# Performance work log

Measured on AMD Instinct MI355X. Metric: run time of the kernel, lower is better.

## Reference

```python
import jax, jax.numpy as jnp
import numpy as np

RCR = 5.2          # radial cutoff
RCA = 3.5          # angular cutoff
ETA_R = 16.0
SHF_R = jnp.asarray(0.9 + 0.26875 * np.arange(16), jnp.float32)          # 16 radial shifts
ZETA = 32.0
SHF_Z = jnp.asarray((2 * np.arange(8) + 1) * np.pi / 16.0, jnp.float32)  # 8 angle shifts
ETA_A = 8.0
SHF_A = jnp.asarray(0.9 + 0.65 * np.arange(4), jnp.float32)              # 4 angular radial shifts
NUM_SPECIES = 4
NUM_PAIRS = NUM_SPECIES * (NUM_SPECIES + 1) // 2  # 10


def _pair_index_table():
    idx = np.zeros((NUM_SPECIES, NUM_SPECIES), np.int32)
    c = 0
    for s1 in range(NUM_SPECIES):
        for s2 in range(s1, NUM_SPECIES):
            idx[s1, s2] = c
            idx[s2, s1] = c
            c += 1
    return jnp.asarray(idx)

PAIR_IDX = _pair_index_table()


def _cutoff(d, rc):
    return jnp.where(d <= rc, 0.5 * jnp.cos(jnp.pi * d / rc) + 0.5, 0.0)


def setup_inputs() -> dict:
    key = jax.random.key(0)
    k1, k2 = jax.random.split(key)
    species = jax.random.randint(k1, (32, 48), 0, NUM_SPECIES, dtype=jnp.int32)
    coords = jax.random.uniform(k2, (32, 48, 3), jnp.float32) * 7.0  # 7 Angstrom box
    return {"species": species, "coords": coords}


def reference(species, coords):
    B, A = species.shape
    dt = coords.dtype
    # vec[b,i,j] = coords[j] - coords[i]
    diff = coords[:, None, :, :] - coords[:, :, None, :]           # [B,A,A,3]
    d2 = jnp.sum(diff * diff, -1)
    eye = jnp.eye(A, dtype=bool)
    dist = jnp.sqrt(jnp.where(eye, 1.0, d2))                        # safe on diagonal
    valid = (species[:, :, None] >= 0) & (species[:, None, :] >= 0) & (~eye)

    # ---------- radial AEV ----------
    fc_r = jnp.where(valid & (dist <= RCR), _cutoff(dist, RCR), 0.0)
    rad_terms = 0.25 * jnp.exp(-ETA_R * (dist[..., None] - SHF_R) ** 2) * fc_r[..., None]  # [B,A,A,16]
    sp_onehot = jax.nn.one_hot(jnp.clip(species, 0), NUM_SPECIES, dtype=dt)                # [B,A,4]
    radial = jnp.einsum('bijr,bjs->bisr', rad_terms, sp_onehot).reshape(B, A, NUM_SPECIES * 16)

    # ---------- angular AEV ----------
    in_ca = valid & (dist <= RCA)
    fc_a = jnp.where(in_ca, _cutoff(dist, RCA), 0.0)
    dotp = jnp.einsum('bijc,bikc->bijk', diff, diff)                # [B,A,A,A]
    cos_t = 0.95 * dotp / (dist[:, :, :, None] * dist[:, :, None, :])
    angles = jnp.arccos(cos_t)
    f1 = ((1.0 + jnp.cos(angles[..., None] - SHF_Z)) * 0.5) ** ZETA          # [B,A,A,A,8]
    avg_d = 0.5 * (dist[:, :, :, None] + dist[:, :, None, :])
    f2 = jnp.exp(-ETA_A * (avg_d[..., None] - SHF_A) ** 2)                   # [B,A,A,A,4]
    jk = jnp.triu(jnp.ones((A, A), bool), 1)                                 # unordered neighbor pairs j<k
    trip_mask = in_ca[:, :, :, None] & in_ca[:, :, None, :] & jk
    w = jnp.where(trip_mask, 2.0 * fc_a[:, :, :, None] * fc_a[:, :, None, :], 0.0)  # [B,A,A,A]
    pair_idx = PAIR_IDX[jnp.clip(species, 0)[:, :, None], jnp.clip(species, 0)[:, None, :]]  # [B,A,A]
    pair_oh = jax.nn.one_hot(pair_idx, NUM_PAIRS, dtype=dt)                  # [B,A,A,10]
    angular = jnp.einsum('bijk,bijka,bijkz,bjkp->bipaz', w, f2, f1, pair_oh)
    angular = angular.reshape(B, A, NUM_PAIRS * 4 * 8)

    aevs = jnp.concatenate([radial, angular], axis=-1)   # [B,A,384]
    return species, aevs
```

## Files before the change

kernel.cpp:

```cpp
#include <hip/hip_runtime.h>
#include <math.h>

#define NB 32
#define NA 48
#define RCRf 5.2f
#define RCAf 3.5f
#define PI_F 3.14159265358979f
#define TREC 1128

typedef unsigned short ushort_t;
typedef __fp16 h2f __attribute__((ext_vector_type(2)));

static __device__ __forceinline__ unsigned pkh(float a, float b) {
    h2f v = __builtin_amdgcn_cvt_pkrtz(a, b);
    return __builtin_bit_cast(unsigned, v);
}
static __device__ __forceinline__ float uph(ushort_t u) {
    return (float)__builtin_bit_cast(__fp16, u);
}

static __device__ __forceinline__ void tri_decode(int t, int m, int T, int& jj, int& kk) {
    const int u = T - 1 - t;
    int r = (int)((sqrtf(8.0f * (float)u + 1.0f) - 1.0f) * 0.5f);
    while (r * (r + 1) / 2 > u) --r;
    while ((r + 1) * (r + 2) / 2 <= u) ++r;
    jj = m - 2 - r;
    kk = m - 1 - (u - r * (r + 1) / 2);
}

__global__ __launch_bounds__(320)
void aev_kernel(const int* __restrict__ species, const float* __restrict__ coords,
                float* __restrict__ out)
{
    const int bid = blockIdx.x;
    const int b = bid / NA;
    const int i = bid - b * NA;
    const int tid = threadIdx.x;

    __shared__ float crd[NA * 3];
    __shared__ int   ssp[NA];
    __shared__ float pd[NA], pfr[NA];
    __shared__ __align__(16) float4 cpk[NA];
    __shared__ float cfc[NA];
    __shared__ int   csp[NA];
    __shared__ int   sm;
    __shared__ float radpart[5 * 64];
    __shared__ __align__(16) ushort_t f1h[TREC * 8];
    __shared__ __align__(16) ushort_t w2h[TREC * 4];
    __shared__ int   cnt[10];
    __shared__ unsigned cur[10];

    if (tid < NA * 3) crd[tid] = coords[(size_t)b * NA * 3 + tid];
    if (tid >= 192 && tid < 192 + NA) ssp[tid - 192] = species[b * NA + (tid - 192)];
    if (tid >= 256 && tid < 266) cnt[tid - 256] = 0;
    __syncthreads();

    const float xi = crd[3 * i], yi = crd[3 * i + 1], zi = crd[3 * i + 2];

    if (tid < 64) {
        const int j = tid;
        float dx = 0.f, dy = 0.f, dz = 0.f, d = 1.0f, fr = 0.0f, fa = 0.0f;
        bool inA = false;
        if (j < NA) {
            dx = crd[3 * j] - xi; dy = crd[3 * j + 1] - yi; dz = crd[3 * j + 2] - zi;
            d = sqrtf(dx * dx + dy * dy + dz * dz);
            if (j != i && d <= RCRf) fr = 0.5f * __cosf((PI_F / RCRf) * d) + 0.5f;
            if (j != i && d <= RCAf) { inA = true; fa = 0.5f * __cosf((PI_F / RCAf) * d) + 0.5f; }
            pd[j] = d; pfr[j] = fr;
        }
        const unsigned long long mask = __ballot(inA);
        if (inA) {
            const int pos = (int)__popcll(mask & ((1ull << j) - 1ull));
            cpk[pos] = make_float4(dx, dy, dz, d);
            cfc[pos] = fa; csp[pos] = ssp[j];
        }
        if (j == 0) sm = (int)__popcll(mask);
    }
    __syncthreads();

    const int m = sm;
    const int T = m * (m - 1) / 2;

    {
        const int f = tid & 63, seg = tid >> 6;
        const int s = f >> 4, r = f & 15;
        const float shf = 0.9f + 0.26875f * (float)r;
        float acc = 0.0f;
        const int j0 = seg * 10, j1 = min(NA, j0 + 10);
        for (int j = j0; j < j1; ++j) {
            const float fr = pfr[j];
            if (fr != 0.0f) {
                const float u = pd[j] - shf;
                const float v = 0.25f * __expf(-16.0f * u * u) * fr;
                acc += (ssp[j] == s) ? v : 0.0f;
            }
        }
        radpart[seg * 64 + f] = acc;
    }
    for (int t = tid; t < T; t += 320) {
        int jj, kk; tri_decode(t, m, T, jj, kk);
        const int s1 = csp[jj], s2 = csp[kk];
        const int lo = min(s1, s2), hi = max(s1, s2);
        const int p = (lo * (9 - lo)) / 2 + (hi - lo);
        atomicAdd(&cnt[p], 1);
    }
    __syncthreads();

    const int pmine = tid >> 5, amine = (tid >> 3) & 3, zmine = tid & 7;
    int mybase = 0, mycnt = 0, run = 0;
    #pragma unroll
    for (int p = 0; p < 10; ++p) {
        const int cp = cnt[p];
        if (p == pmine) { mybase = run; mycnt = cp; }
        if (tid < 10 && p == tid) cur[tid] = (unsigned)run;
        run += cp;
    }
    __syncthreads();

    const float CZ[8] = { 0.98078528f, 0.83146961f, 0.55557023f, 0.19509032f,
                         -0.19509032f,-0.55557023f,-0.83146961f,-0.98078528f };
    const float SZ[8] = { 0.19509032f, 0.55557023f, 0.83146961f, 0.98078528f,
                          0.98078528f, 0.83146961f, 0.55557023f, 0.19509032f };
    const float SA[4] = { 0.9f, 1.55f, 2.2f, 2.85f };

    for (int t = tid; t < T; t += 320) {
        int jj, kk; tri_decode(t, m, T, jj, kk);
        const float4 qj = cpk[jj];
        const float4 qk = cpk[kk];
        const float dot = qj.x * qk.x + qj.y * qk.y + qj.z * qk.z;
        const float cosT = 0.95f * dot * __frcp_rn(qj.w * qk.w);
        const float sinT = sqrtf(fmaxf(1.0f - cosT * cosT, 0.0f));
        const float avg = 0.5f * (qj.w + qk.w);
        const float w = 2.0f * cfc[jj] * cfc[kk];
        const int s1 = csp[jj], s2 = csp[kk];
        const int lo = min(s1, s2), hi = max(s1, s2);
        const int p = (lo * (9 - lo)) / 2 + (hi - lo);

        float f1v[8];
        #pragma unroll
        for (int z = 0; z < 8; ++z) {
            const float base = 0.5f + 0.5f * (cosT * CZ[z] + sinT * SZ[z]);
            const float b2 = base * base, b4 = b2 * b2, b8 = b4 * b4, b16 = b8 * b8;
            f1v[z] = b16 * b16;
        }
        float w2v[4];
        #pragma unroll
        for (int a = 0; a < 4; ++a) {
            const float u = avg - SA[a];
            w2v[a] = w * __expf(-8.0f * u * u);
        }
        const unsigned pos = atomicAdd(&cur[p], 1u);
        uint4 rf;
        rf.x = pkh(f1v[0], f1v[1]); rf.y = pkh(f1v[2], f1v[3]);
        rf.z = pkh(f1v[4], f1v[5]); rf.w = pkh(f1v[6], f1v[7]);
        ((uint4*)f1h)[pos] = rf;
        uint2 rw;
        rw.x = pkh(w2v[0], w2v[1]); rw.y = pkh(w2v[2], w2v[3]);
        ((uint2*)w2h)[pos] = rw;
    }
    __syncthreads();

    float acc_a = 0.0f;
    for (int k = mybase; k < mybase + mycnt; ++k)
        acc_a += uph(w2h[k * 4 + amine]) * uph(f1h[k * 8 + zmine]);

    float* op = out + NB * NA + (size_t)(b * NA + i) * 384;
    if (tid < 64) {
        op[tid] = radpart[tid] + radpart[64 + tid] + radpart[128 + tid] +
                  radpart[192 + tid] + radpart[256 + tid];
    }
    op[64 + tid] = acc_a;
    if (tid == 0) out[b * NA + i] = (float)ssp[i];
}

extern "C" void kernel_launch(void* const* d_in, const int* in_sizes, int n_in,
                              void* d_out, int out_size, void* d_ws, size_t ws_size,
                              hipStream_t stream) {
    const int*   species = (const int*)d_in[0];
    const float* coords  = (const float*)d_in[1];
    float*       out     = (float*)d_out;
    aev_kernel<<<NB * NA, 320, 0, stream>>>(species, coords, out);
}
```

Before: 66.03 us.

## Store compact per-triplet records and compute angular terms in consumer threads

The counting pass, prefix sum and atomic bucketing by species pair are removed. Each triplet now writes a compact record (cosT, sinT, fp16 avg/weight, pair id) indexed by triplet number. Each output thread scans every record and evaluates only those matching its pair, computing its own angle and radial term. Coordinates and species are also read straight from global memory instead of being staged in shared memory. This drops atomics and a barrier but makes every thread scan all T records. It also recomputes exp and the power chain per output element, and adds fp16 rounding of the average distance.

```diff
diff --git a/kernel.cpp b/kernel.cpp
--- a/kernel.cpp
+++ b/kernel.cpp
@@ -6,17 +6,12 @@
 #define RCRf 5.2f
 #define RCAf 3.5f
 #define PI_F 3.14159265358979f
-#define TREC 1128
+#define TREC 1081
 
-typedef unsigned short ushort_t;
 typedef __fp16 h2f __attribute__((ext_vector_type(2)));
-
 static __device__ __forceinline__ unsigned pkh(float a, float b) {
     h2f v = __builtin_amdgcn_cvt_pkrtz(a, b);
     return __builtin_bit_cast(unsigned, v);
-}
-static __device__ __forceinline__ float uph(ushort_t u) {
-    return (float)__builtin_bit_cast(__fp16, u);
 }
 
 static __device__ __forceinline__ void tri_decode(int t, int m, int T, int& jj, int& kk) {
@@ -37,42 +32,35 @@
     const int i = bid - b * NA;
     const int tid = threadIdx.x;
 
-    __shared__ float crd[NA * 3];
+    __shared__ float pd[NA], pfr[NA];
     __shared__ int   ssp[NA];
-    __shared__ float pd[NA], pfr[NA];
     __shared__ __align__(16) float4 cpk[NA];
     __shared__ float cfc[NA];
     __shared__ int   csp[NA];
     __shared__ int   sm;
     __shared__ float radpart[5 * 64];
-    __shared__ __align__(16) ushort_t f1h[TREC * 8];
-    __shared__ __align__(16) ushort_t w2h[TREC * 4];
-    __shared__ int   cnt[10];
-    __shared__ unsigned cur[10];
-
-    if (tid < NA * 3) crd[tid] = coords[(size_t)b * NA * 3 + tid];
-    if (tid >= 192 && tid < 192 + NA) ssp[tid - 192] = species[b * NA + (tid - 192)];
-    if (tid >= 256 && tid < 266) cnt[tid - 256] = 0;
-    __syncthreads();
-
-    const float xi = crd[3 * i], yi = crd[3 * i + 1], zi = crd[3 * i + 2];
+    __shared__ __align__(16) uint4 rec[TREC];
 
     if (tid < 64) {
         const int j = tid;
         float dx = 0.f, dy = 0.f, dz = 0.f, d = 1.0f, fr = 0.0f, fa = 0.0f;
+        int sj = 0;
         bool inA = false;
         if (j < NA) {
-            dx = crd[3 * j] - xi; dy = crd[3 * j + 1] - yi; dz = crd[3 * j + 2] - zi;
+            const float* cb = coords + (size_t)b * NA * 3;
+            const float xi = cb[3 * i], yi = cb[3 * i + 1], zi = cb[3 * i + 2];
+            dx = cb[3 * j] - xi; dy = cb[3 * j + 1] - yi; dz = cb[3 * j + 2] - zi;
             d = sqrtf(dx * dx + dy * dy + dz * dz);
+            sj = species[b * NA + j];
             if (j != i && d <= RCRf) fr = 0.5f * __cosf((PI_F / RCRf) * d) + 0.5f;
             if (j != i && d <= RCAf) { inA = true; fa = 0.5f * __cosf((PI_F / RCAf) * d) + 0.5f; }
-            pd[j] = d; pfr[j] = fr;
+            pd[j] = d; pfr[j] = fr; ssp[j] = sj;
         }
         const unsigned long long mask = __ballot(inA);
         if (inA) {
             const int pos = (int)__popcll(mask & ((1ull << j) - 1ull));
             cpk[pos] = make_float4(dx, dy, dz, d);
-            cfc[pos] = fa; csp[pos] = ssp[j];
+            cfc[pos] = fa; csp[pos] = sj;
         }
         if (j == 0) sm = (int)__popcll(mask);
     }
@@ -97,31 +85,6 @@
         }
         radpart[seg * 64 + f] = acc;
     }
-    for (int t = tid; t < T; t += 320) {
-        int jj, kk; tri_decode(t, m, T, jj, kk);
-        const int s1 = csp[jj], s2 = csp[kk];
-        const int lo = min(s1, s2), hi = max(s1, s2);
-        const int p = (lo * (9 - lo)) / 2 + (hi - lo);
-        atomicAdd(&cnt[p], 1);
-    }
-    __syncthreads();
-
-    const int pmine = tid >> 5, amine = (tid >> 3) & 3, zmine = tid & 7;
-    int mybase = 0, mycnt = 0, run = 0;
-    #pragma unroll
-    for (int p = 0; p < 10; ++p) {
-        const int cp = cnt[p];
-        if (p == pmine) { mybase = run; mycnt = cp; }
-        if (tid < 10 && p == tid) cur[tid] = (unsigned)run;
-        run += cp;
-    }
-    __syncthreads();
-
-    const float CZ[8] = { 0.98078528f, 0.83146961f, 0.55557023f, 0.19509032f,
-                         -0.19509032f,-0.55557023f,-0.83146961f,-0.98078528f };
-    const float SZ[8] = { 0.19509032f, 0.55557023f, 0.83146961f, 0.98078528f,
-                          0.98078528f, 0.83146961f, 0.55557023f, 0.19509032f };
-    const float SA[4] = { 0.9f, 1.55f, 2.2f, 2.85f };
 
     for (int t = tid; t < T; t += 320) {
         int jj, kk; tri_decode(t, m, T, jj, kk);
@@ -135,34 +98,36 @@
         const int s1 = csp[jj], s2 = csp[kk];
         const int lo = min(s1, s2), hi = max(s1, s2);
         const int p = (lo * (9 - lo)) / 2 + (hi - lo);
-
-        float f1v[8];
-        #pragma unroll
-        for (int z = 0; z < 8; ++z) {
-            const float base = 0.5f + 0.5f * (cosT * CZ[z] + sinT * SZ[z]);
-            const float b2 = base * base, b4 = b2 * b2, b8 = b4 * b4, b16 = b8 * b8;
-            f1v[z] = b16 * b16;
-        }
-        float w2v[4];
-        #pragma unroll
-        for (int a = 0; a < 4; ++a) {
-            const float u = avg - SA[a];
-            w2v[a] = w * __expf(-8.0f * u * u);
-        }
-        const unsigned pos = atomicAdd(&cur[p], 1u);
-        uint4 rf;
-        rf.x = pkh(f1v[0], f1v[1]); rf.y = pkh(f1v[2], f1v[3]);
-        rf.z = pkh(f1v[4], f1v[5]); rf.w = pkh(f1v[6], f1v[7]);
-        ((uint4*)f1h)[pos] = rf;
-        uint2 rw;
-        rw.x = pkh(w2v[0], w2v[1]); rw.y = pkh(w2v[2], w2v[3]);
-        ((uint2*)w2h)[pos] = rw;
+        uint4 r;
+        r.x = __float_as_uint(cosT);
+        r.y = __float_as_uint(sinT);
+        r.z = pkh(avg, w);
+        r.w = (unsigned)p;
+        rec[t] = r;
     }
     __syncthreads();
 
+    const int pmine = tid >> 5;
+    const float CZt[8] = { 0.98078528f, 0.83146961f, 0.55557023f, 0.19509032f,
+                          -0.19509032f,-0.55557023f,-0.83146961f,-0.98078528f };
+    const float SZt[8] = { 0.19509032f, 0.55557023f, 0.83146961f, 0.98078528f,
+                           0.98078528f, 0.83146961f, 0.55557023f, 0.19509032f };
+    const float cz = CZt[tid & 7], sz = SZt[tid & 7];
+    const float sa = 0.9f + 0.65f * (float)((tid >> 3) & 3);
     float acc_a = 0.0f;
-    for (int k = mybase; k < mybase + mycnt; ++k)
-        acc_a += uph(w2h[k * 4 + amine]) * uph(f1h[k * 8 + zmine]);
+    for (int t = 0; t < T; ++t) {
+        const uint4 r = rec[t];
+        if ((int)r.w == pmine) {
+            const float cosT = __uint_as_float(r.x);
+            const float sinT = __uint_as_float(r.y);
+            const h2f aw = __builtin_bit_cast(h2f, r.z);
+            const float avg = (float)aw.x, w = (float)aw.y;
+            const float base = 0.5f + 0.5f * (cosT * cz + sinT * sz);
+            const float b2 = base * base, b4 = b2 * b2, b8 = b4 * b4, b16 = b8 * b8;
+            const float u = avg - sa;
+            acc_a += w * __expf(-8.0f * u * u) * (b16 * b16);
+        }
+    }
 
     float* op = out + NB * NA + (size_t)(b * NA + i) * 384;
     if (tid < 64) {
```

Result: slower. 88.22 us (+33.6%).

## Chunk triplet staging buffer and load coords directly from global

Applied to the files above, without the earlier changes.

The per-block LDS staging buffer for triplet features now has a fixed size and is processed in chunks, so a neighbour count of any size no longer overflows it. The smaller buffer also lowers LDS use per block, which may let more blocks share a CU. The initial copy of coordinates and species into LDS, and the barrier after it, are removed; each thread reads its own values straight from global memory. Multi-chunk cases add extra barriers and a second counting pass.

```diff
diff --git a/kernel.cpp b/kernel.cpp
--- a/kernel.cpp
+++ b/kernel.cpp
@@ -6,11 +6,10 @@
 #define RCRf 5.2f
 #define RCAf 3.5f
 #define PI_F 3.14159265358979f
-#define TREC 1128
+#define CMAX 1000
 
 typedef unsigned short ushort_t;
 typedef __fp16 h2f __attribute__((ext_vector_type(2)));
-
 static __device__ __forceinline__ unsigned pkh(float a, float b) {
     h2f v = __builtin_amdgcn_cvt_pkrtz(a, b);
     return __builtin_bit_cast(unsigned, v);
@@ -37,42 +36,40 @@
     const int i = bid - b * NA;
     const int tid = threadIdx.x;
 
-    __shared__ float crd[NA * 3];
+    __shared__ float pd[NA], pfr[NA];
     __shared__ int   ssp[NA];
-    __shared__ float pd[NA], pfr[NA];
     __shared__ __align__(16) float4 cpk[NA];
     __shared__ float cfc[NA];
     __shared__ int   csp[NA];
     __shared__ int   sm;
     __shared__ float radpart[5 * 64];
-    __shared__ __align__(16) ushort_t f1h[TREC * 8];
-    __shared__ __align__(16) ushort_t w2h[TREC * 4];
+    __shared__ __align__(16) ushort_t f1h[CMAX * 8];
+    __shared__ __align__(16) ushort_t w2h[CMAX * 4];
     __shared__ int   cnt[10];
     __shared__ unsigned cur[10];
 
-    if (tid < NA * 3) crd[tid] = coords[(size_t)b * NA * 3 + tid];
-    if (tid >= 192 && tid < 192 + NA) ssp[tid - 192] = species[b * NA + (tid - 192)];
     if (tid >= 256 && tid < 266) cnt[tid - 256] = 0;
-    __syncthreads();
-
-    const float xi = crd[3 * i], yi = crd[3 * i + 1], zi = crd[3 * i + 2];
 
     if (tid < 64) {
         const int j = tid;
         float dx = 0.f, dy = 0.f, dz = 0.f, d = 1.0f, fr = 0.0f, fa = 0.0f;
+        int sj = 0;
         bool inA = false;
         if (j < NA) {
-            dx = crd[3 * j] - xi; dy = crd[3 * j + 1] - yi; dz = crd[3 * j + 2] - zi;
+            const float* cb = coords + (size_t)b * NA * 3;
+            const float xi = cb[3 * i], yi = cb[3 * i + 1], zi = cb[3 * i + 2];
+            dx = cb[3 * j] - xi; dy = cb[3 * j + 1] - yi; dz = cb[3 * j + 2] - zi;
             d = sqrtf(dx * dx + dy * dy + dz * dz);
+            sj = species[b * NA + j];
             if (j != i && d <= RCRf) fr = 0.5f * __cosf((PI_F / RCRf) * d) + 0.5f;
             if (j != i && d <= RCAf) { inA = true; fa = 0.5f * __cosf((PI_F / RCAf) * d) + 0.5f; }
-            pd[j] = d; pfr[j] = fr;
+            pd[j] = d; pfr[j] = fr; ssp[j] = sj;
         }
         const unsigned long long mask = __ballot(inA);
         if (inA) {
             const int pos = (int)__popcll(mask & ((1ull << j) - 1ull));
             cpk[pos] = make_float4(dx, dy, dz, d);
-            cfc[pos] = fa; csp[pos] = ssp[j];
+            cfc[pos] = fa; csp[pos] = sj;
         }
         if (j == 0) sm = (int)__popcll(mask);
     }
@@ -80,6 +77,7 @@
 
     const int m = sm;
     const int T = m * (m - 1) / 2;
+    const int nchunks = (T + CMAX - 1) / CMAX;
 
     {
         const int f = tid & 63, seg = tid >> 6;
@@ -97,72 +95,96 @@
         }
         radpart[seg * 64 + f] = acc;
     }
-    for (int t = tid; t < T; t += 320) {
-        int jj, kk; tri_decode(t, m, T, jj, kk);
-        const int s1 = csp[jj], s2 = csp[kk];
-        const int lo = min(s1, s2), hi = max(s1, s2);
-        const int p = (lo * (9 - lo)) / 2 + (hi - lo);
-        atomicAdd(&cnt[p], 1);
+    {
+        const int cT = min(CMAX, T);
+        for (int t = tid; t < cT; t += 320) {
+            int jj, kk; tri_decode(t, m, T, jj, kk);
+            const int s1 = csp[jj], s2 = csp[kk];
+            const int lo = min(s1, s2), hi = max(s1, s2);
+            const int p = (lo * (9 - lo)) / 2 + (hi - lo);
+            atomicAdd(&cnt[p], 1);
+        }
     }
     __syncthreads();
 
     const int pmine = tid >> 5, amine = (tid >> 3) & 3, zmine = tid & 7;
-    int mybase = 0, mycnt = 0, run = 0;
-    #pragma unroll
-    for (int p = 0; p < 10; ++p) {
-        const int cp = cnt[p];
-        if (p == pmine) { mybase = run; mycnt = cp; }
-        if (tid < 10 && p == tid) cur[tid] = (unsigned)run;
-        run += cp;
-    }
-    __syncthreads();
-
     const float CZ[8] = { 0.98078528f, 0.83146961f, 0.55557023f, 0.19509032f,
                          -0.19509032f,-0.55557023f,-0.83146961f,-0.98078528f };
     const float SZ[8] = { 0.19509032f, 0.55557023f, 0.83146961f, 0.98078528f,
                           0.98078528f, 0.83146961f, 0.55557023f, 0.19509032f };
     const float SA[4] = { 0.9f, 1.55f, 2.2f, 2.85f };
-
-    for (int t = tid; t < T; t += 320) {
-        int jj, kk; tri_decode(t, m, T, jj, kk);
-        const float4 qj = cpk[jj];
-        const float4 qk = cpk[kk];
-        const float dot = qj.x * qk.x + qj.y * qk.y + qj.z * qk.z;
-        const float cosT = 0.95f * dot * __frcp_rn(qj.w * qk.w);
-        const float sinT = sqrtf(fmaxf(1.0f - cosT * cosT, 0.0f));
-        const float avg = 0.5f * (qj.w + qk.w);
-        const float w = 2.0f * cfc[jj] * cfc[kk];
-        const int s1 = csp[jj], s2 = csp[kk];
-        const int lo = min(s1, s2), hi = max(s1, s2);
-        const int p = (lo * (9 - lo)) / 2 + (hi - lo);
-
-        float f1v[8];
+    float acc_a = 0.0f;
+
+    for (int c = 0; c < nchunks; ++c) {
+        const int t0 = c * CMAX;
+        const int cT = min(CMAX, T - t0);
+
+        int mybase = 0, mycnt = 0, run = 0;
         #pragma unroll
-        for (int z = 0; z < 8; ++z) {
-            const float base = 0.5f + 0.5f * (cosT * CZ[z] + sinT * SZ[z]);
-            const float b2 = base * base, b4 = b2 * b2, b8 = b4 * b4, b16 = b8 * b8;
-            f1v[z] = b16 * b16;
-        }
-        float w2v[4];
-        #pragma unroll
-        for (int a = 0; a < 4; ++a) {
-            const float u = avg - SA[a];
-            w2v[a] = w * __expf(-8.0f * u * u);
-        }
-        const unsigned pos = atomicAdd(&cur[p], 1u);
-        uint4 rf;
-        rf.x = pkh(f1v[0], f1v[1]); rf.y = pkh(f1v[2], f1v[3]);
-        rf.z = pkh(f1v[4], f1v[5]); rf.w = pkh(f1v[6], f1v[7]);
-        ((uint4*)f1h)[pos] = rf;
-        uint2 rw;
-        rw.x = pkh(w2v[0], w2v[1]); rw.y = pkh(w2v[2], w2v[3]);
-        ((uint2*)w2h)[pos] = rw;
-    }
-    __syncthreads();
-
-    float acc_a = 0.0f;
-    for (int k = mybase; k < mybase + mycnt; ++k)
-        acc_a += uph(w2h[k * 4 + amine]) * uph(f1h[k * 8 + zmine]);
+        for (int p = 0; p < 10; ++p) {
+            const int cp = cnt[p];
+            if (p == pmine) { mybase = run; mycnt = cp; }
+            if (tid < 10 && p == tid) cur[tid] = (unsigned)run;
+            run += cp;
+        }
+        __syncthreads();
+
+        for (int t = tid; t < cT; t += 320) {
+            int jj, kk; tri_decode(t0 + t, m, T, jj, kk);
+            const float4 qj = cpk[jj];
+            const float4 qk = cpk[kk];
+            const float dot = qj.x * qk.x + qj.y * qk.y + qj.z * qk.z;
+            const float cosT = 0.95f * dot * __frcp_rn(qj.w * qk.w);
+            const float sinT = sqrtf(fmaxf(1.0f - cosT * cosT, 0.0f));
+            const float avg = 0.5f * (qj.w + qk.w);
+            const float w = 2.0f * cfc[jj] * cfc[kk];
+            const int s1 = csp[jj], s2 = csp[kk];
+            const int lo = min(s1, s2), hi = max(s1, s2);
+            const int p = (lo * (9 - lo)) / 2 + (hi - lo);
+
+            float f1v[8];
+            #pragma unroll
+            for (int z = 0; z < 8; ++z) {
+                const float base = 0.5f + 0.5f * (cosT * CZ[z] + sinT * SZ[z]);
+                const float b2 = base * base, b4 = b2 * b2, b8 = b4 * b4, b16 = b8 * b8;
+                f1v[z] = b16 * b16;
+            }
+            float w2v[4];
+            #pragma unroll
+            for (int a = 0; a < 4; ++a) {
+                const float u = avg - SA[a];
+                w2v[a] = w * __expf(-8.0f * u * u);
+            }
+            const unsigned pos = atomicAdd(&cur[p], 1u);
+            uint4 rf;
+            rf.x = pkh(f1v[0], f1v[1]); rf.y = pkh(f1v[2], f1v[3]);
+            rf.z = pkh(f1v[4], f1v[5]); rf.w = pkh(f1v[6], f1v[7]);
+            ((uint4*)f1h)[pos] = rf;
+            uint2 rw;
+            rw.x = pkh(w2v[0], w2v[1]); rw.y = pkh(w2v[2], w2v[3]);
+            ((uint2*)w2h)[pos] = rw;
+        }
+        __syncthreads();
+
+        for (int k = mybase; k < mybase + mycnt; ++k)
+            acc_a += uph(w2h[k * 4 + amine]) * uph(f1h[k * 8 + zmine]);
+
+        if (c + 1 < nchunks) {
+            __syncthreads();
+            if (tid < 10) cnt[tid] = 0;
+            __syncthreads();
+            const int n0 = (c + 1) * CMAX;
+            const int nT = min(CMAX, T - n0);
+            for (int t = tid; t < nT; t += 320) {
+                int jj, kk; tri_decode(n0 + t, m, T, jj, kk);
+                const int s1 = csp[jj], s2 = csp[kk];
+                const int lo = min(s1, s2), hi = max(s1, s2);
+                const int p = (lo * (9 - lo)) / 2 + (hi - lo);
+                atomicAdd(&cnt[p], 1);
+            }
+            __syncthreads();
+        }
+    }
 
     float* op = out + NB * NA + (size_t)(b * NA + i) * 384;
     if (tid < 64) {
```

New measurement: 65.55 us. No clear change (-0.7%).
